# Kernel tuning notes

Hardware: AMD Instinct MI355X
Metric: run time of the kernel (lower is better)

## Reference

```python
import jax, jax.numpy as jnp
import numpy as np

POLY = jnp.array([-0.037, 0.481, -2.3, 4.917, -1.791], dtype=jnp.float32)


def adaptive_temperature_softmax(logits):
    # logits: [b, h, n, n]
    p = jax.nn.softmax(logits, axis=-1)
    entropy = jnp.sum(-p * jnp.log(p + 1e-9), axis=-1, keepdims=True)  # [b,h,n,1]
    poly = (POLY[0] * entropy**4 + POLY[1] * entropy**3
            + POLY[2] * entropy**2 + POLY[3] * entropy + POLY[4])
    beta = jnp.where(entropy > 0.5, jnp.maximum(poly, 1.0), 1.0)
    return jax.nn.softmax(logits * beta, axis=-1)


def setup_inputs() -> dict:
    key = jax.random.key(0)
    ks = jax.random.split(key, 5)
    b, n, dim = 2, 2048, 1024
    s = 0.02
    return {
        "x": jax.random.normal(ks[0], (b, n, dim), dtype=jnp.float32),
        "Wq": jax.random.normal(ks[1], (dim, dim), dtype=jnp.float32) * s,
        "Wk": jax.random.normal(ks[2], (dim, dim), dtype=jnp.float32) * s,
        "Wv": jax.random.normal(ks[3], (dim, dim), dtype=jnp.float32) * s,
        "Wo": jax.random.normal(ks[4], (dim, dim), dtype=jnp.float32) * s,
        "bo": jnp.zeros((dim,), dtype=jnp.float32),
    }


def reference(x, Wq, Wk, Wv, Wo, bo):
    b, n, dim = x.shape
    h = 16
    hd = dim // h

    def split_heads(t):  # [b,n,dim] -> [b,h,n,hd]
        return t.reshape(b, n, h, hd).transpose(0, 2, 1, 3)

    # torch Linear: y = x @ W.T
    q = split_heads(x @ Wq.T)
    k = split_heads(x @ Wk.T)
    v = split_heads(x @ Wv.T)

    sim = jnp.einsum('bhid,bhjd->bhij', q, k) / jnp.sqrt(jnp.float32(hd))
    causal = jnp.triu(jnp.ones((n, n), dtype=bool), 1)
    neg = -jnp.finfo(sim.dtype).max
    sim = jnp.where(causal, neg, sim)

    attn = adaptive_temperature_softmax(sim)
    out = jnp.einsum('bhij,bhjd->bhid', attn, v)
    out = out.transpose(0, 2, 1, 3).reshape(b, n, dim)
    return out @ Wo.T + bo
```

## Files before the change

### kernel.cpp

```cpp
#include <hip/hip_runtime.h>
#include <hip/hip_bf16.h>

typedef __attribute__((ext_vector_type(8))) short bf16x8;
typedef __attribute__((ext_vector_type(4))) short short4v;
typedef __attribute__((ext_vector_type(4))) float f32x4;
typedef unsigned int u32;

__device__ __forceinline__ short f2bf(float f) {
    union { float f; u32 i; } c; c.f = f;
    u32 r = c.i + 0x7FFFu + ((c.i >> 16) & 1u);
    return (short)(r >> 16);
}
__device__ __forceinline__ u32 pack2bf(float lo, float hi) {
    return ((u32)(unsigned short)f2bf(hi) << 16) | (u32)(unsigned short)f2bf(lo);
}
__device__ __forceinline__ f32x4 mfma16(bf16x8 a, bf16x8 b, f32x4 c) {
    return __builtin_amdgcn_mfma_f32_16x16x32_bf16(a, b, c, 0, 0, 0);
}
__device__ __forceinline__ f32x4 mfma16k16(short4v a, short4v b, f32x4 c) {
#if __has_builtin(__builtin_amdgcn_mfma_f32_16x16x16bf16_1k)
    return __builtin_amdgcn_mfma_f32_16x16x16bf16_1k(a, b, c, 0, 0, 0);
#else
    f32x4 d = c;
    asm volatile("v_mfma_f32_16x16x16_bf16 %0, %1, %2, %0"
                 : "+v"(d) : "v"(a), "v"(b));
    return d;
#endif
}
__device__ __forceinline__ void load_lds16(const void* g, void* l) {
    __builtin_amdgcn_global_load_lds(
        (const __attribute__((address_space(1))) u32*)g,
        (__attribute__((address_space(3))) u32*)l, 16, 0, 0);
}

__global__ __launch_bounds__(256) void cvt_all_kernel(
    const float* __restrict__ x, const float* __restrict__ wq,
    const float* __restrict__ wk, const float* __restrict__ wv,
    const float* __restrict__ wo, short* __restrict__ ws) {
    const int XV = (4096 * 1024) / 4;
    const int WV = (1024 * 1024) / 4;
    int i = blockIdx.x * 256 + threadIdx.x;
    const float4* src; short4v* dst; int off;
    if (i < XV)            { src = (const float4*)x;  dst = (short4v*)(ws);           off = i; }
    else if (i < XV + WV)  { src = (const float4*)wq; dst = (short4v*)(ws + 4194304); off = i - XV; }
    else if (i < XV + 2*WV){ src = (const float4*)wk; dst = (short4v*)(ws + 5242880); off = i - XV - WV; }
    else if (i < XV + 3*WV){ src = (const float4*)wv; dst = (short4v*)(ws + 6291456); off = i - XV - 2*WV; }
    else                   { src = (const float4*)wo; dst = (short4v*)(ws + 7340032); off = i - XV - 3*WV; }
    float4 v = src[off];
    short4v o;
    o.x = f2bf(v.x); o.y = f2bf(v.y); o.z = f2bf(v.z); o.w = f2bf(v.w);
    dst[off] = o;
}

__device__ __forceinline__ void gemm_mainloop(
    const short* __restrict__ A, const short* __restrict__ Bm,
    short* lds, int mbase, int nbase, int wave, int lane, f32x4 acc[4][4]) {
    const int K = 1024;
    const int lr = lane & 15, lg = lane >> 4;
    const int wm = wave >> 1, wn = wave & 1;
    for (int k0 = 0; k0 < K; k0 += 64) {
        __syncthreads();
        #pragma unroll
        for (int issue = 0; issue < 4; ++issue) {
            int f = issue * 4 + wave;
            int mt = f >> 1, kc = f & 1;
            load_lds16(A  + (size_t)(mbase + mt*16 + lr)*K + (k0 + kc*32 + lg*8), lds + f*512);
            load_lds16(Bm + (size_t)(nbase + mt*16 + lr)*K + (k0 + kc*32 + lg*8), lds + 8192 + f*512);
        }
        __syncthreads();
        #pragma unroll
        for (int kc = 0; kc < 2; ++kc) {
            bf16x8 af[4], bfv[4];
            #pragma unroll
            for (int mi = 0; mi < 4; ++mi)
                af[mi] = *(const bf16x8*)(lds + ((wm*4 + mi)*2 + kc)*512 + lane*8);
            #pragma unroll
            for (int ni = 0; ni < 4; ++ni)
                bfv[ni] = *(const bf16x8*)(lds + 8192 + ((wn*4 + ni)*2 + kc)*512 + lane*8);
            #pragma unroll
            for (int mi = 0; mi < 4; ++mi)
                #pragma unroll
                for (int ni = 0; ni < 4; ++ni)
                    acc[mi][ni] = mfma16(af[mi], bfv[ni], acc[mi][ni]);
        }
    }
}

__global__ __launch_bounds__(256) void gemm_qkv_kernel(
    const short* __restrict__ xb, const short* __restrict__ wqb,
    const short* __restrict__ wkb, const short* __restrict__ wvb,
    short* __restrict__ Qh, short* __restrict__ Kh, short* __restrict__ Vf) {
    __shared__ short lds[16896];
    const int wave = threadIdx.x >> 6, lane = threadIdx.x & 63;
    const int lr = lane & 15, lg = lane >> 4;
    const int sel = blockIdx.x >> 3;
    const int nbase = (blockIdx.x & 7) * 128;
    const int mbase = blockIdx.y * 128;
    const short* Bm = (sel == 0) ? wqb : (sel == 1) ? wkb : wvb;

    f32x4 acc[4][4];
    #pragma unroll
    for (int i = 0; i < 4; ++i)
        #pragma unroll
        for (int j = 0; j < 4; ++j) acc[i][j] = f32x4{0.f, 0.f, 0.f, 0.f};

    gemm_mainloop(xb, Bm, lds, mbase, nbase, wave, lane, acc);

    const int wm = wave >> 1, wn = wave & 1;
    if (sel == 2) {
        #pragma unroll
        for (int mi = 0; mi < 4; ++mi) {
            int m0 = mbase + wm*64 + mi*16 + lg*4;
            #pragma unroll
            for (int ni = 0; ni < 4; ++ni) {
                int nc = nbase + wn*64 + ni*16 + lr;
                int h = nc >> 6, d = nc & 63;
                f32x4 v = acc[mi][ni];
                int bi = m0 >> 11, np = m0 & 2047;
                int c = np >> 6, s = (np >> 4) & 3, lg2 = (np >> 2) & 3;
                int dc = d >> 4, lr2 = d & 15;
                size_t off = ((size_t)(bi*16 + h)*32 + c)*4096
                           + (size_t)((s*4 + dc)*64 + lg2*16 + lr2)*4;
                short4v o;
                o.x = f2bf(v.x); o.y = f2bf(v.y); o.z = f2bf(v.z); o.w = f2bf(v.w);
                *(short4v*)&Vf[off] = o;
            }
        }
    } else {
        short* dstb = (sel == 0) ? Qh : Kh;
        const float sc = (sel == 0) ? 0.125f : 1.0f;
        __syncthreads();
        #pragma unroll
        for (int mi = 0; mi < 4; ++mi) {
            int row0 = wm*64 + mi*16 + lg*4;
            #pragma unroll
            for (int ni = 0; ni < 4; ++ni) {
                int col = wn*64 + ni*16 + lr;
                f32x4 v = acc[mi][ni];
                #pragma unroll
                for (int r = 0; r < 4; ++r)
                    lds[(row0 + r)*132 + col] = f2bf(v[r] * sc);
            }
        }
        __syncthreads();
        const int h0 = nbase >> 6;
        const int tid = threadIdx.x;
        #pragma unroll
        for (int it = 0; it < 8; ++it) {
            int L = it*256 + tid;
            int np_l = L >> 4;
            int t16 = L & 15;
            int P = t16 >> 3;
            int c8 = (t16 & 7) * 8;
            bf16x8 val = *(const bf16x8*)&lds[np_l*132 + P*64 + c8];
            int m = mbase + np_l; int bi = m >> 11, np = m & 2047;
            *(bf16x8*)&dstb[((size_t)(bi*16 + h0 + P)*2048 + np)*64 + c8] = val;
        }
    }
}

__global__ __launch_bounds__(256) void gemm_out_kernel(
    const short* __restrict__ AO, const short* __restrict__ wob,
    const float* __restrict__ bias, float* __restrict__ out) {
    __shared__ short lds[12288];
    const int K = 1024;
    const int wave = threadIdx.x >> 6, lane = threadIdx.x & 63;
    const int lr = lane & 15, lg = lane >> 4;
    const int nbase = blockIdx.x * 128;
    const int mbase = blockIdx.y * 64;
    const int wm = wave >> 1, wn = wave & 1;

    f32x4 acc[2][4];
    #pragma unroll
    for (int i = 0; i < 2; ++i)
        #pragma unroll
        for (int j = 0; j < 4; ++j) acc[i][j] = f32x4{0.f, 0.f, 0.f, 0.f};

    for (int k0 = 0; k0 < K; k0 += 64) {
        __syncthreads();
        #pragma unroll
        for (int l = 0; l < 6; ++l) {
            int f = l*4 + wave;
            if (f < 8) {
                int mt = f >> 1, kc = f & 1;
                load_lds16(AO + (size_t)(mbase + mt*16 + lr)*K + (k0 + kc*32 + lg*8),
                           lds + f*512);
            } else {
                int fb = f - 8, nt = fb >> 1, kc = fb & 1;
                load_lds16(wob + (size_t)(nbase + nt*16 + lr)*K + (k0 + kc*32 + lg*8),
                           lds + 4096 + fb*512);
            }
        }
        __syncthreads();
        #pragma unroll
        for (int kc = 0; kc < 2; ++kc) {
            bf16x8 af[2], bfv[4];
            #pragma unroll
            for (int mi = 0; mi < 2; ++mi)
                af[mi] = *(const bf16x8*)(lds + ((wm*2 + mi)*2 + kc)*512 + lane*8);
            #pragma unroll
            for (int ni = 0; ni < 4; ++ni)
                bfv[ni] = *(const bf16x8*)(lds + 4096 + ((wn*4 + ni)*2 + kc)*512 + lane*8);
            #pragma unroll
            for (int mi = 0; mi < 2; ++mi)
                #pragma unroll
                for (int ni = 0; ni < 4; ++ni)
                    acc[mi][ni] = mfma16(af[mi], bfv[ni], acc[mi][ni]);
        }
    }

    #pragma unroll
    for (int mi = 0; mi < 2; ++mi) {
        int m0 = mbase + wm*32 + mi*16 + lg*4;
        #pragma unroll
        for (int ni = 0; ni < 4; ++ni) {
            int nc = nbase + wn*64 + ni*16 + lr;
            float bj = bias[nc];
            f32x4 v = acc[mi][ni];
            #pragma unroll
            for (int r = 0; r < 4; ++r)
                out[(size_t)(m0 + r)*1024 + nc] = v[r] + bj;
        }
    }
}

__global__ __launch_bounds__(256, 4) void attn_kernel(
    const short* __restrict__ Qh, const short* __restrict__ Kh,
    const short* __restrict__ Vf, short* __restrict__ AO) {
    __shared__ short lds[16384];
    const int lane = threadIdx.x & 63;
    const int wave = threadIdx.x >> 6;
    const int lr = lane & 15, lg = lane >> 4;
    const int bid  = blockIdx.x;
    const int xcd  = bid & 7;
    const int rest = bid >> 3;
    const int u    = 31 - (rest >> 2);
    const int bh   = ((rest & 3) << 3) | xcd;
    const int b = bh >> 4, h = bh & 15;
    const int qbase = u*64 + wave*16;
    const int qa = qbase + lr;
    const short* Q  = Qh + (size_t)bh * (2048 * 64);
    const short* Kg = Kh + (size_t)bh * (2048 * 64);
    const short* Vg = Vf + (size_t)bh * (32 * 4096);

    bf16x8 qf0 = *(const bf16x8*)&Q[(size_t)qa*64 + lg*8];
    bf16x8 qf1 = *(const bf16x8*)&Q[(size_t)qa*64 + 32 + lg*8];

    const int fc0 = wave * 2;

    auto stageK = [&](int buf, int c) {
        #pragma unroll
        for (int i = 0; i < 2; ++i) {
            int fc = fc0 + i, s = fc >> 1, ch = fc & 1;
            load_lds16(Kg + ((size_t)(c*64 + s*16 + lr)*64 + ch*32 + lg*8),
                       &lds[buf*4096 + fc*512]);
        }
    };
    auto stageV = [&](int buf, int c) {
        #pragma unroll
        for (int i = 0; i < 2; ++i) {
            int fi = fc0 + i;
            load_lds16(Vg + (size_t)c*4096 + fi*512 + lane*8,
                       &lds[8192 + buf*4096 + fi*512]);
        }
    };

    float sm = 0.f, tm = 0.f;
    stageK(0, 0);
    #pragma unroll 1
    for (int c = 0; c <= u; ++c) {
        __syncthreads();
        if (c < u) stageK((c + 1) & 1, c + 1);
        const int base = (c & 1) * 4096;
        #pragma unroll
        for (int s = 0; s < 4; ++s) {
            int k0 = c*64 + s*16;
            if (k0 <= qbase) {
                bf16x8 kf0 = *(const bf16x8*)&lds[base + (s*2    )*512 + lane*8];
                bf16x8 kf1 = *(const bf16x8*)&lds[base + (s*2 + 1)*512 + lane*8];
                f32x4 d = {0.f,0.f,0.f,0.f};
                d = mfma16(kf0, qf0, d); d = mfma16(kf1, qf1, d);
                if (k0 < qbase) {
                    #pragma unroll
                    for (int r = 0; r < 4; ++r) {
                        float e = __expf(d[r]); sm += e; tm += e * d[r];
                    }
                } else {
                    int kb = k0 + lg*4;
                    #pragma unroll
                    for (int r = 0; r < 4; ++r) {
                        float l = (kb + r <= qa) ? d[r] : -1e30f;
                        float e = __expf(l); sm += e; tm += e * l;
                    }
                }
            }
        }
    }
    sm += __shfl_xor(sm, 16); tm += __shfl_xor(tm, 16);
    sm += __shfl_xor(sm, 32); tm += __shfl_xor(tm, 32);
    float H = __logf(sm) - tm / sm;
    float beta = 1.f;
    if (H > 0.5f)
        beta = fmaxf((((-0.037f*H + 0.481f)*H - 2.3f)*H + 4.917f)*H - 1.791f, 1.f);

    f32x4 o0 = {0.f,0.f,0.f,0.f}, o1 = {0.f,0.f,0.f,0.f};
    f32x4 o2 = {0.f,0.f,0.f,0.f}, o3 = {0.f,0.f,0.f,0.f};
    float s2 = 0.f;
    __syncthreads();
    stageK(0, 0); stageV(0, 0);
    #pragma unroll 1
    for (int c = 0; c <= u; ++c) {
        __syncthreads();
        if (c < u) { stageK((c + 1) & 1, c + 1); stageV((c + 1) & 1, c + 1); }
        const int kb_ = (c & 1) * 4096;
        const int vb_ = 8192 + (c & 1) * 4096;
        #pragma unroll
        for (int s = 0; s < 4; ++s) {
            int k0 = c*64 + s*16;
            if (k0 <= qbase) {
                bf16x8 kf0 = *(const bf16x8*)&lds[kb_ + (s*2    )*512 + lane*8];
                bf16x8 kf1 = *(const bf16x8*)&lds[kb_ + (s*2 + 1)*512 + lane*8];
                f32x4 d = {0.f,0.f,0.f,0.f};
                d = mfma16(kf0, qf0, d); d = mfma16(kf1, qf1, d);
                float pv[4];
                if (k0 < qbase) {
                    #pragma unroll
                    for (int r = 0; r < 4; ++r) { pv[r] = __expf(beta * d[r]); s2 += pv[r]; }
                } else {
                    int kb = k0 + lg*4;
                    #pragma unroll
                    for (int r = 0; r < 4; ++r) {
                        pv[r] = (kb + r <= qa) ? __expf(beta * d[r]) : 0.f; s2 += pv[r];
                    }
                }
                union { short4v s4; u32 uu[2]; } pb;
                pb.uu[0] = pack2bf(pv[0], pv[1]);
                pb.uu[1] = pack2bf(pv[2], pv[3]);
                short4v vf0 = *(const short4v*)&lds[vb_ + ((s*4 + 0)*64 + lane)*4];
                short4v vf1 = *(const short4v*)&lds[vb_ + ((s*4 + 1)*64 + lane)*4];
                short4v vf2 = *(const short4v*)&lds[vb_ + ((s*4 + 2)*64 + lane)*4];
                short4v vf3 = *(const short4v*)&lds[vb_ + ((s*4 + 3)*64 + lane)*4];
                o0 = mfma16k16(vf0, pb.s4, o0);
                o1 = mfma16k16(vf1, pb.s4, o1);
                o2 = mfma16k16(vf2, pb.s4, o2);
                o3 = mfma16k16(vf3, pb.s4, o3);
            }
        }
    }
    s2 += __shfl_xor(s2, 16); s2 += __shfl_xor(s2, 32);
    float inv = 1.f / s2;

    size_t row = ((size_t)(b*2048 + qa))*1024 + h*64;
    f32x4 oo[4] = {o0, o1, o2, o3};
    #pragma unroll
    for (int dc = 0; dc < 4; ++dc) {
        short4v wv;
        #pragma unroll
        for (int r = 0; r < 4; ++r) wv[r] = f2bf(oo[dc][r] * inv);
        *(short4v*)&AO[row + dc*16 + lg*4] = wv;
    }
}

extern "C" void kernel_launch(void* const* d_in, const int* in_sizes, int n_in,
                              void* d_out, int out_size, void* d_ws, size_t ws_size,
                              hipStream_t stream) {
    const float* x  = (const float*)d_in[0];
    const float* Wq = (const float*)d_in[1];
    const float* Wk = (const float*)d_in[2];
    const float* Wv = (const float*)d_in[3];
    const float* Wo = (const float*)d_in[4];
    const float* bo = (const float*)d_in[5];
    float* out = (float*)d_out;
    short* ws = (short*)d_ws;

    short* xb  = ws;
    short* wqb = ws + 4194304;
    short* wkb = ws + 5242880;
    short* wvb = ws + 6291456;
    short* wob = ws + 7340032;
    short* Qh  = ws + 8388608;
    short* Kh  = ws + 12582912;
    short* Vf  = ws + 16777216;
    short* AO  = ws + 20971520;

    cvt_all_kernel<<<8192, 256, 0, stream>>>(x, Wq, Wk, Wv, Wo, ws);
    gemm_qkv_kernel<<<dim3(24, 32), 256, 0, stream>>>(xb, wqb, wkb, wvb, Qh, Kh, Vf);
    attn_kernel<<<1024, 256, 0, stream>>>(Qh, Kh, Vf, AO);
    gemm_out_kernel<<<dim3(8, 64), 256, 0, stream>>>(AO, wob, bo, out);
}
```

Before: 158.2 us.

## Pair causal query tiles per attention block, shrink QKV GEMM tile, use exp2

The attention kernel now runs 2-wave blocks that each handle two 32-row query tiles from opposite ends of the causal triangle, so every block does a similar amount of work and K/V tiles staged in LDS serve both tiles. The QKV GEMM tile shrinks from 128x128 to 64x128, doubling the grid and allowing more resident blocks. Softmax exponentials switch to native exp2, with log2(e) folded into the Q scale and the entropy rescaled by ln2. The trade-off is more register pressure from the doubled accumulators in attention and less operand reuse per GEMM block.

```diff
diff --git a/kernel.cpp b/kernel.cpp
--- a/kernel.cpp
+++ b/kernel.cpp
@@ -25,6 +25,13 @@
     asm volatile("v_mfma_f32_16x16x16_bf16 %0, %1, %2, %0"
                  : "+v"(d) : "v"(a), "v"(b));
     return d;
+#endif
+}
+__device__ __forceinline__ float fexp2(float x) {
+#if __has_builtin(__builtin_amdgcn_exp2f)
+    return __builtin_amdgcn_exp2f(x);
+#else
+    float r; asm("v_exp_f32 %0, %1" : "=v"(r) : "v"(x)); return r;
 #endif
 }
 __device__ __forceinline__ void load_lds16(const void* g, void* l) {
@@ -52,65 +59,63 @@
     dst[off] = o;
 }
 
-__device__ __forceinline__ void gemm_mainloop(
-    const short* __restrict__ A, const short* __restrict__ Bm,
-    short* lds, int mbase, int nbase, int wave, int lane, f32x4 acc[4][4]) {
-    const int K = 1024;
-    const int lr = lane & 15, lg = lane >> 4;
-    const int wm = wave >> 1, wn = wave & 1;
-    for (int k0 = 0; k0 < K; k0 += 64) {
-        __syncthreads();
-        #pragma unroll
-        for (int issue = 0; issue < 4; ++issue) {
-            int f = issue * 4 + wave;
-            int mt = f >> 1, kc = f & 1;
-            load_lds16(A  + (size_t)(mbase + mt*16 + lr)*K + (k0 + kc*32 + lg*8), lds + f*512);
-            load_lds16(Bm + (size_t)(nbase + mt*16 + lr)*K + (k0 + kc*32 + lg*8), lds + 8192 + f*512);
-        }
-        __syncthreads();
-        #pragma unroll
-        for (int kc = 0; kc < 2; ++kc) {
-            bf16x8 af[4], bfv[4];
-            #pragma unroll
-            for (int mi = 0; mi < 4; ++mi)
-                af[mi] = *(const bf16x8*)(lds + ((wm*4 + mi)*2 + kc)*512 + lane*8);
-            #pragma unroll
-            for (int ni = 0; ni < 4; ++ni)
-                bfv[ni] = *(const bf16x8*)(lds + 8192 + ((wn*4 + ni)*2 + kc)*512 + lane*8);
-            #pragma unroll
-            for (int mi = 0; mi < 4; ++mi)
-                #pragma unroll
-                for (int ni = 0; ni < 4; ++ni)
-                    acc[mi][ni] = mfma16(af[mi], bfv[ni], acc[mi][ni]);
-        }
-    }
-}
-
-__global__ __launch_bounds__(256) void gemm_qkv_kernel(
+__global__ __launch_bounds__(256, 6) void gemm_qkv_kernel(
     const short* __restrict__ xb, const short* __restrict__ wqb,
     const short* __restrict__ wkb, const short* __restrict__ wvb,
     short* __restrict__ Qh, short* __restrict__ Kh, short* __restrict__ Vf) {
-    __shared__ short lds[16896];
+    __shared__ short lds[12288];
+    const int K = 1024;
     const int wave = threadIdx.x >> 6, lane = threadIdx.x & 63;
     const int lr = lane & 15, lg = lane >> 4;
     const int sel = blockIdx.x >> 3;
     const int nbase = (blockIdx.x & 7) * 128;
-    const int mbase = blockIdx.y * 128;
+    const int mbase = blockIdx.y * 64;
     const short* Bm = (sel == 0) ? wqb : (sel == 1) ? wkb : wvb;
-
-    f32x4 acc[4][4];
+    const int wm = wave >> 1, wn = wave & 1;
+
+    f32x4 acc[2][4];
     #pragma unroll
-    for (int i = 0; i < 4; ++i)
+    for (int i = 0; i < 2; ++i)
         #pragma unroll
         for (int j = 0; j < 4; ++j) acc[i][j] = f32x4{0.f, 0.f, 0.f, 0.f};
 
-    gemm_mainloop(xb, Bm, lds, mbase, nbase, wave, lane, acc);
-
-    const int wm = wave >> 1, wn = wave & 1;
+    for (int k0 = 0; k0 < K; k0 += 64) {
+        __syncthreads();
+        #pragma unroll
+        for (int l = 0; l < 6; ++l) {
+            int f = l*4 + wave;
+            if (f < 8) {
+                int mt = f >> 1, kc = f & 1;
+                load_lds16(xb + (size_t)(mbase + mt*16 + lr)*K + (k0 + kc*32 + lg*8),
+                           lds + f*512);
+            } else {
+                int fb = f - 8, nt = fb >> 1, kc = fb & 1;
+                load_lds16(Bm + (size_t)(nbase + nt*16 + lr)*K + (k0 + kc*32 + lg*8),
+                           lds + 4096 + fb*512);
+            }
+        }
+        __syncthreads();
+        #pragma unroll
+        for (int kc = 0; kc < 2; ++kc) {
+            bf16x8 af[2], bfv[4];
+            #pragma unroll
+            for (int mi = 0; mi < 2; ++mi)
+                af[mi] = *(const bf16x8*)(lds + ((wm*2 + mi)*2 + kc)*512 + lane*8);
+            #pragma unroll
+            for (int ni = 0; ni < 4; ++ni)
+                bfv[ni] = *(const bf16x8*)(lds + 4096 + ((wn*4 + ni)*2 + kc)*512 + lane*8);
+            #pragma unroll
+            for (int mi = 0; mi < 2; ++mi)
+                #pragma unroll
+                for (int ni = 0; ni < 4; ++ni)
+                    acc[mi][ni] = mfma16(af[mi], bfv[ni], acc[mi][ni]);
+        }
+    }
+
     if (sel == 2) {
         #pragma unroll
-        for (int mi = 0; mi < 4; ++mi) {
-            int m0 = mbase + wm*64 + mi*16 + lg*4;
+        for (int mi = 0; mi < 2; ++mi) {
+            int m0 = mbase + wm*32 + mi*16 + lg*4;
             #pragma unroll
             for (int ni = 0; ni < 4; ++ni) {
                 int nc = nbase + wn*64 + ni*16 + lr;
@@ -128,11 +133,11 @@
         }
     } else {
         short* dstb = (sel == 0) ? Qh : Kh;
-        const float sc = (sel == 0) ? 0.125f : 1.0f;
-        __syncthreads();
-        #pragma unroll
-        for (int mi = 0; mi < 4; ++mi) {
-            int row0 = wm*64 + mi*16 + lg*4;
+        const float sc = (sel == 0) ? 0.125f * 1.44269504f : 1.0f;
+        __syncthreads();
+        #pragma unroll
+        for (int mi = 0; mi < 2; ++mi) {
+            int row0 = wm*32 + mi*16 + lg*4;
             #pragma unroll
             for (int ni = 0; ni < 4; ++ni) {
                 int col = wn*64 + ni*16 + lr;
@@ -146,10 +151,10 @@
         const int h0 = nbase >> 6;
         const int tid = threadIdx.x;
         #pragma unroll
-        for (int it = 0; it < 8; ++it) {
-            int L = it*256 + tid;
-            int np_l = L >> 4;
-            int t16 = L & 15;
+        for (int it = 0; it < 4; ++it) {
+            int g = it*256 + tid;
+            int np_l = g >> 4;
+            int t16 = g & 15;
             int P = t16 >> 3;
             int c8 = (t16 & 7) * 8;
             bf16x8 val = *(const bf16x8*)&lds[np_l*132 + P*64 + c8];
@@ -224,7 +229,7 @@
     }
 }
 
-__global__ __launch_bounds__(256, 4) void attn_kernel(
+__global__ __launch_bounds__(128) void attn_kernel(
     const short* __restrict__ Qh, const short* __restrict__ Kh,
     const short* __restrict__ Vf, short* __restrict__ AO) {
     __shared__ short lds[16384];
@@ -234,23 +239,27 @@
     const int bid  = blockIdx.x;
     const int xcd  = bid & 7;
     const int rest = bid >> 3;
-    const int u    = 31 - (rest >> 2);
+    const int pr   = rest >> 2;
     const int bh   = ((rest & 3) << 3) | xcd;
     const int b = bh >> 4, h = bh & 15;
-    const int qbase = u*64 + wave*16;
-    const int qa = qbase + lr;
+    const int tA = 63 - pr, tB = pr;
+    const int qbA = tA*32 + wave*16, qaA = qbA + lr;
+    const int qbB = tB*32 + wave*16, qaB = qbB + lr;
+    const int u2 = tA >> 1;
     const short* Q  = Qh + (size_t)bh * (2048 * 64);
     const short* Kg = Kh + (size_t)bh * (2048 * 64);
     const short* Vg = Vf + (size_t)bh * (32 * 4096);
 
-    bf16x8 qf0 = *(const bf16x8*)&Q[(size_t)qa*64 + lg*8];
-    bf16x8 qf1 = *(const bf16x8*)&Q[(size_t)qa*64 + 32 + lg*8];
-
-    const int fc0 = wave * 2;
+    bf16x8 qfA0 = *(const bf16x8*)&Q[(size_t)qaA*64 + lg*8];
+    bf16x8 qfA1 = *(const bf16x8*)&Q[(size_t)qaA*64 + 32 + lg*8];
+    bf16x8 qfB0 = *(const bf16x8*)&Q[(size_t)qaB*64 + lg*8];
+    bf16x8 qfB1 = *(const bf16x8*)&Q[(size_t)qaB*64 + 32 + lg*8];
+
+    const int fc0 = wave * 4;
 
     auto stageK = [&](int buf, int c) {
         #pragma unroll
-        for (int i = 0; i < 2; ++i) {
+        for (int i = 0; i < 4; ++i) {
             int fc = fc0 + i, s = fc >> 1, ch = fc & 1;
             load_lds16(Kg + ((size_t)(c*64 + s*16 + lr)*64 + ch*32 + lg*8),
                        &lds[buf*4096 + fc*512]);
@@ -258,106 +267,159 @@
     };
     auto stageV = [&](int buf, int c) {
         #pragma unroll
-        for (int i = 0; i < 2; ++i) {
+        for (int i = 0; i < 4; ++i) {
             int fi = fc0 + i;
             load_lds16(Vg + (size_t)c*4096 + fi*512 + lane*8,
                        &lds[8192 + buf*4096 + fi*512]);
         }
     };
 
-    float sm = 0.f, tm = 0.f;
+    float sA = 0.f, t2A = 0.f, sB = 0.f, t2B = 0.f;
     stageK(0, 0);
     #pragma unroll 1
-    for (int c = 0; c <= u; ++c) {
-        __syncthreads();
-        if (c < u) stageK((c + 1) & 1, c + 1);
+    for (int c = 0; c <= u2; ++c) {
+        __syncthreads();
+        if (c < u2) stageK((c + 1) & 1, c + 1);
         const int base = (c & 1) * 4096;
         #pragma unroll
         for (int s = 0; s < 4; ++s) {
-            int k0 = c*64 + s*16;
-            if (k0 <= qbase) {
-                bf16x8 kf0 = *(const bf16x8*)&lds[base + (s*2    )*512 + lane*8];
-                bf16x8 kf1 = *(const bf16x8*)&lds[base + (s*2 + 1)*512 + lane*8];
-                f32x4 d = {0.f,0.f,0.f,0.f};
-                d = mfma16(kf0, qf0, d); d = mfma16(kf1, qf1, d);
-                if (k0 < qbase) {
+            const int k0 = c*64 + s*16;
+            if (k0 > qbA) continue;
+            bf16x8 kf0 = *(const bf16x8*)&lds[base + (s*2    )*512 + lane*8];
+            bf16x8 kf1 = *(const bf16x8*)&lds[base + (s*2 + 1)*512 + lane*8];
+            f32x4 d = {0.f,0.f,0.f,0.f};
+            d = mfma16(kf0, qfA0, d); d = mfma16(kf1, qfA1, d);
+            if (k0 < qbA) {
+                #pragma unroll
+                for (int r = 0; r < 4; ++r) {
+                    float e = fexp2(d[r]); sA += e; t2A += e * d[r];
+                }
+            } else {
+                int kb = k0 + lg*4;
+                #pragma unroll
+                for (int r = 0; r < 4; ++r) {
+                    float dd = (kb + r <= qaA) ? d[r] : -1e30f;
+                    float e = fexp2(dd); sA += e; t2A += e * dd;
+                }
+            }
+            if (k0 <= qbB) {
+                f32x4 d2 = {0.f,0.f,0.f,0.f};
+                d2 = mfma16(kf0, qfB0, d2); d2 = mfma16(kf1, qfB1, d2);
+                if (k0 < qbB) {
                     #pragma unroll
                     for (int r = 0; r < 4; ++r) {
-                        float e = __expf(d[r]); sm += e; tm += e * d[r];
+                        float e = fexp2(d2[r]); sB += e; t2B += e * d2[r];
                     }
                 } else {
                     int kb = k0 + lg*4;
                     #pragma unroll
                     for (int r = 0; r < 4; ++r) {
-                        float l = (kb + r <= qa) ? d[r] : -1e30f;
-                        float e = __expf(l); sm += e; tm += e * l;
+                        float dd = (kb + r <= qaB) ? d2[r] : -1e30f;
+                        float e = fexp2(dd); sB += e; t2B += e * dd;
                     }
                 }
             }
         }
     }
-    sm += __shfl_xor(sm, 16); tm += __shfl_xor(tm, 16);
-    sm += __shfl_xor(sm, 32); tm += __shfl_xor(tm, 32);
-    float H = __logf(sm) - tm / sm;
-    float beta = 1.f;
-    if (H > 0.5f)
-        beta = fmaxf((((-0.037f*H + 0.481f)*H - 2.3f)*H + 4.917f)*H - 1.791f, 1.f);
-
-    f32x4 o0 = {0.f,0.f,0.f,0.f}, o1 = {0.f,0.f,0.f,0.f};
-    f32x4 o2 = {0.f,0.f,0.f,0.f}, o3 = {0.f,0.f,0.f,0.f};
-    float s2 = 0.f;
+    sA += __shfl_xor(sA, 16); t2A += __shfl_xor(t2A, 16);
+    sA += __shfl_xor(sA, 32); t2A += __shfl_xor(t2A, 32);
+    sB += __shfl_xor(sB, 16); t2B += __shfl_xor(t2B, 16);
+    sB += __shfl_xor(sB, 32); t2B += __shfl_xor(t2B, 32);
+    const float LN2 = 0.69314718f;
+    float HA = LN2 * (__log2f(sA) - t2A / sA);
+    float HB = LN2 * (__log2f(sB) - t2B / sB);
+    float betaA = 1.f, betaB = 1.f;
+    if (HA > 0.5f)
+        betaA = fmaxf((((-0.037f*HA + 0.481f)*HA - 2.3f)*HA + 4.917f)*HA - 1.791f, 1.f);
+    if (HB > 0.5f)
+        betaB = fmaxf((((-0.037f*HB + 0.481f)*HB - 2.3f)*HB + 4.917f)*HB - 1.791f, 1.f);
+
+    f32x4 oA0 = {0.f,0.f,0.f,0.f}, oA1 = {0.f,0.f,0.f,0.f};
+    f32x4 oA2 = {0.f,0.f,0.f,0.f}, oA3 = {0.f,0.f,0.f,0.f};
+    f32x4 oB0 = {0.f,0.f,0.f,0.f}, oB1 = {0.f,0.f,0.f,0.f};
+    f32x4 oB2 = {0.f,0.f,0.f,0.f}, oB3 = {0.f,0.f,0.f,0.f};
+    float s2A = 0.f, s2B = 0.f;
     __syncthreads();
     stageK(0, 0); stageV(0, 0);
     #pragma unroll 1
-    for (int c = 0; c <= u; ++c) {
-        __syncthreads();
-        if (c < u) { stageK((c + 1) & 1, c + 1); stageV((c + 1) & 1, c + 1); }
+    for (int c = 0; c <= u2; ++c) {
+        __syncthreads();
+        if (c < u2) { stageK((c + 1) & 1, c + 1); stageV((c + 1) & 1, c + 1); }
         const int kb_ = (c & 1) * 4096;
         const int vb_ = 8192 + (c & 1) * 4096;
         #pragma unroll
         for (int s = 0; s < 4; ++s) {
-            int k0 = c*64 + s*16;
-            if (k0 <= qbase) {
-                bf16x8 kf0 = *(const bf16x8*)&lds[kb_ + (s*2    )*512 + lane*8];
-                bf16x8 kf1 = *(const bf16x8*)&lds[kb_ + (s*2 + 1)*512 + lane*8];
-                f32x4 d = {0.f,0.f,0.f,0.f};
-                d = mfma16(kf0, qf0, d); d = mfma16(kf1, qf1, d);
-                float pv[4];
-                if (k0 < qbase) {
+            const int k0 = c*64 + s*16;
+            if (k0 > qbA) continue;
+            bf16x8 kf0 = *(const bf16x8*)&lds[kb_ + (s*2    )*512 + lane*8];
+            bf16x8 kf1 = *(const bf16x8*)&lds[kb_ + (s*2 + 1)*512 + lane*8];
+            short4v vf0 = *(const short4v*)&lds[vb_ + ((s*4 + 0)*64 + lane)*4];
+            short4v vf1 = *(const short4v*)&lds[vb_ + ((s*4 + 1)*64 + lane)*4];
+            short4v vf2 = *(const short4v*)&lds[vb_ + ((s*4 + 2)*64 + lane)*4];
+            short4v vf3 = *(const short4v*)&lds[vb_ + ((s*4 + 3)*64 + lane)*4];
+            f32x4 d = {0.f,0.f,0.f,0.f};
+            d = mfma16(kf0, qfA0, d); d = mfma16(kf1, qfA1, d);
+            float pv[4];
+            if (k0 < qbA) {
+                #pragma unroll
+                for (int r = 0; r < 4; ++r) { pv[r] = fexp2(betaA * d[r]); s2A += pv[r]; }
+            } else {
+                int kb = k0 + lg*4;
+                #pragma unroll
+                for (int r = 0; r < 4; ++r) {
+                    float dd = (kb + r <= qaA) ? d[r] : -1e30f;
+                    pv[r] = fexp2(betaA * dd); s2A += pv[r];
+                }
+            }
+            union { short4v s4; u32 uu[2]; } pb;
+            pb.uu[0] = pack2bf(pv[0], pv[1]);
+            pb.uu[1] = pack2bf(pv[2], pv[3]);
+            oA0 = mfma16k16(vf0, pb.s4, oA0);
+            oA1 = mfma16k16(vf1, pb.s4, oA1);
+            oA2 = mfma16k16(vf2, pb.s4, oA2);
+            oA3 = mfma16k16(vf3, pb.s4, oA3);
+            if (k0 <= qbB) {
+                f32x4 d2 = {0.f,0.f,0.f,0.f};
+                d2 = mfma16(kf0, qfB0, d2); d2 = mfma16(kf1, qfB1, d2);
+                if (k0 < qbB) {
                     #pragma unroll
-                    for (int r = 0; r < 4; ++r) { pv[r] = __expf(beta * d[r]); s2 += pv[r]; }
+                    for (int r = 0; r < 4; ++r) { pv[r] = fexp2(betaB * d2[r]); s2B += pv[r]; }
                 } else {
                     int kb = k0 + lg*4;
                     #pragma unroll
                     for (int r = 0; r < 4; ++r) {
-                        pv[r] = (kb + r <= qa) ? __expf(beta * d[r]) : 0.f; s2 += pv[r];
+                        float dd = (kb + r <= qaB) ? d2[r] : -1e30f;
+                        pv[r] = fexp2(betaB * dd); s2B += pv[r];
                     }
                 }
-                union { short4v s4; u32 uu[2]; } pb;
-                pb.uu[0] = pack2bf(pv[0], pv[1]);
-                pb.uu[1] = pack2bf(pv[2], pv[3]);
-                short4v vf0 = *(const short4v*)&lds[vb_ + ((s*4 + 0)*64 + lane)*4];
-                short4v vf1 = *(const short4v*)&lds[vb_ + ((s*4 + 1)*64 + lane)*4];
-                short4v vf2 = *(const short4v*)&lds[vb_ + ((s*4 + 2)*64 + lane)*4];
-                short4v vf3 = *(const short4v*)&lds[vb_ + ((s*4 + 3)*64 + lane)*4];
-                o0 = mfma16k16(vf0, pb.s4, o0);
-                o1 = mfma16k16(vf1, pb.s4, o1);
-                o2 = mfma16k16(vf2, pb.s4, o2);
-                o3 = mfma16k16(vf3, pb.s4, o3);
-            }
-        }
-    }
-    s2 += __shfl_xor(s2, 16); s2 += __shfl_xor(s2, 32);
-    float inv = 1.f / s2;
-
-    size_t row = ((size_t)(b*2048 + qa))*1024 + h*64;
-    f32x4 oo[4] = {o0, o1, o2, o3};
+                union { short4v s4; u32 uu[2]; } pb2;
+                pb2.uu[0] = pack2bf(pv[0], pv[1]);
+                pb2.uu[1] = pack2bf(pv[2], pv[3]);
+                oB0 = mfma16k16(vf0, pb2.s4, oB0);
+                oB1 = mfma16k16(vf1, pb2.s4, oB1);
+                oB2 = mfma16k16(vf2, pb2.s4, oB2);
+                oB3 = mfma16k16(vf3, pb2.s4, oB3);
+            }
+        }
+    }
+    s2A += __shfl_xor(s2A, 16); s2A += __shfl_xor(s2A, 32);
+    s2B += __shfl_xor(s2B, 16); s2B += __shfl_xor(s2B, 32);
+    float invA = 1.f / s2A, invB = 1.f / s2B;
+
+    size_t rowA = ((size_t)(b*2048 + qaA))*1024 + h*64;
+    size_t rowB = ((size_t)(b*2048 + qaB))*1024 + h*64;
+    f32x4 ooA[4] = {oA0, oA1, oA2, oA3};
+    f32x4 ooB[4] = {oB0, oB1, oB2, oB3};
     #pragma unroll
     for (int dc = 0; dc < 4; ++dc) {
-        short4v wv;
-        #pragma unroll
-        for (int r = 0; r < 4; ++r) wv[r] = f2bf(oo[dc][r] * inv);
-        *(short4v*)&AO[row + dc*16 + lg*4] = wv;
+        short4v wa, wb;
+        #pragma unroll
+        for (int r = 0; r < 4; ++r) {
+            wa[r] = f2bf(ooA[dc][r] * invA);
+            wb[r] = f2bf(ooB[dc][r] * invB);
+        }
+        *(short4v*)&AO[rowA + dc*16 + lg*4] = wa;
+        *(short4v*)&AO[rowB + dc*16 + lg*4] = wb;
     }
 }
 
@@ -384,7 +446,7 @@
     short* AO  = ws + 20971520;
 
     cvt_all_kernel<<<8192, 256, 0, stream>>>(x, Wq, Wk, Wv, Wo, ws);
-    gemm_qkv_kernel<<<dim3(24, 32), 256, 0, stream>>>(xb, wqb, wkb, wvb, Qh, Kh, Vf);
-    attn_kernel<<<1024, 256, 0, stream>>>(Qh, Kh, Vf, AO);
+    gemm_qkv_kernel<<<dim3(24, 64), 256, 0, stream>>>(xb, wqb, wkb, wvb, Qh, Kh, Vf);
+    attn_kernel<<<1024, 128, 0, stream>>>(Qh, Kh, Vf, AO);
     gemm_out_kernel<<<dim3(8, 64), 256, 0, stream>>>(AO, wob, bo, out);
 }
```

After: 226.0 us. +42.9%, slower.
